# Kernel tuning notes

Hardware: AMD Instinct MI355X
Metric: run time of the kernel (lower is better)

## Reference

```python
import jax, jax.numpy as jnp
import numpy as np

H = 16          # num_attention_heads
D_MODEL = 2048  # hidden_size
HEAD_DIM = D_MODEL // H  # 128
B, S = 4, 2048


def setup_inputs() -> dict:
    key = jax.random.key(0)
    ks = jax.random.split(key, 9)
    std = D_MODEL ** -0.5
    hidden_states = jax.random.normal(ks[0], (B, S, D_MODEL), dtype=jnp.float32)
    q_w = jax.random.normal(ks[1], (H * HEAD_DIM, D_MODEL), dtype=jnp.float32) * std
    k_w = jax.random.normal(ks[2], (HEAD_DIM, D_MODEL), dtype=jnp.float32) * std
    v_w = jax.random.normal(ks[3], (HEAD_DIM, D_MODEL), dtype=jnp.float32) * std
    o_w = jax.random.normal(ks[4], (D_MODEL, H * HEAD_DIM), dtype=jnp.float32) * std
    q_b = jnp.zeros((H * HEAD_DIM,), dtype=jnp.float32)
    k_b = jnp.zeros((HEAD_DIM,), dtype=jnp.float32)
    v_b = jnp.zeros((HEAD_DIM,), dtype=jnp.float32)
    o_b = jnp.zeros((D_MODEL,), dtype=jnp.float32)
    return {"hidden_states": hidden_states, "q_w": q_w, "q_b": q_b,
            "k_w": k_w, "k_b": k_b, "v_w": v_w, "v_b": v_b,
            "o_w": o_w, "o_b": o_b}


def reference(hidden_states, q_w, q_b, k_w, k_b, v_w, v_b, o_w, o_b):
    b, s, _ = hidden_states.shape
    # projections: q -> H heads, k/v -> single shared KV head (MQA)
    q = (hidden_states @ q_w.T + q_b).reshape(b, s, H, HEAD_DIM)   # bshd
    k = hidden_states @ k_w.T + k_b                                 # bkd (1 kv head)
    v = hidden_states @ v_w.T + v_b                                 # bkd
    # QK^T with KV head broadcast across all query heads
    scores = jnp.einsum('bqhd,bkd->bhqk', q, k) / (HEAD_DIM ** 0.5)
    # causal mask (triu above diagonal)
    causal = jnp.triu(jnp.ones((s, s), dtype=bool), k=1)
    scores = jnp.where(causal[None, None], -jnp.inf, scores)
    # softmax in fp32, cast back to input dtype
    attn = jax.nn.softmax(scores.astype(jnp.float32), axis=-1).astype(q.dtype)
    out = jnp.einsum('bhqk,bkd->bqhd', attn, v).reshape(b, s, H * HEAD_DIM)
    return out @ o_w.T + o_b
```

## Files before the change

### kernel.cpp

```cpp
#include <hip/hip_runtime.h>
#include <stdint.h>

typedef __bf16 bf16;
typedef __bf16 bf16x4 __attribute__((ext_vector_type(4)));
typedef __bf16 bf16x8 __attribute__((ext_vector_type(8)));
typedef float f32x4 __attribute__((ext_vector_type(4)));
typedef short s16x4 __attribute__((ext_vector_type(4)));

using gp_t = __attribute__((address_space(1))) const void*;
using lp_t = __attribute__((address_space(3))) void*;

__device__ __forceinline__ void gld16(const void* g, void* l) {
  __builtin_amdgcn_global_load_lds((gp_t)g, (lp_t)l, 16, 0, 0);
}

struct CvtSegs {
  const float* src[10];
  bf16* dst[10];
  int cnt[10];
  int n;
};

__global__ void cvt_kernel(CvtSegs segs) {
  const int stride = gridDim.x * blockDim.x;
  const int t0 = blockIdx.x * blockDim.x + threadIdx.x;
  for (int s = 0; s < segs.n; s++) {
    const float4* src = (const float4*)segs.src[s];
    bf16x4* dst = (bf16x4*)segs.dst[s];
    int cnt4 = segs.cnt[s] >> 2;
    for (int idx = t0; idx < cnt4; idx += stride) {
      float4 v = src[idx];
      bf16x4 o; o[0] = (bf16)v.x; o[1] = (bf16)v.y; o[2] = (bf16)v.z; o[3] = (bf16)v.w;
      dst[idx] = o;
    }
  }
}

__global__ __launch_bounds__(256, 2)
void gemm_bt(const bf16* __restrict__ A, const void* __restrict__ Wv,
             const void* __restrict__ biasv, void* __restrict__ Cv,
             void* __restrict__ Cv2, void* __restrict__ Cv3,
             int M, int N, int K, int w_fp32, int bias_fp32, int store_sel)
{
  __shared__ __align__(16) bf16 As[128 * 64];
  __shared__ __align__(16) bf16 Bs[128 * 64];
  const int tid  = threadIdx.x;
  const int lane = tid & 63;
  const int w    = tid >> 6;
  const int wm   = w >> 1, wn = w & 1;
  const int quad = lane >> 4, l16 = lane & 15;
  const int m0 = blockIdx.x * 128, n0 = blockIdx.y * 128;

  f32x4 acc[4][4] = {};

  for (int k0 = 0; k0 < K; k0 += 64) {
#pragma unroll
    for (int it = 0; it < 4; it++) {
      int c = tid + it * 256;
      int row = c >> 3;
      int cc  = (c & 7) ^ (row & 7);
      gld16(A + (size_t)(m0 + row) * K + k0 + cc * 8, &As[c * 8]);
      size_t woff = (size_t)(n0 + row) * K + k0 + cc * 8;
      if (!w_fp32) {
        gld16((const bf16*)Wv + woff, &Bs[c * 8]);
      } else {
        const float* Wf = (const float*)Wv;
        float4 x0 = *(const float4*)(Wf + woff);
        float4 x1 = *(const float4*)(Wf + woff + 4);
        bf16x8 v;
        v[0] = (bf16)x0.x; v[1] = (bf16)x0.y; v[2] = (bf16)x0.z; v[3] = (bf16)x0.w;
        v[4] = (bf16)x1.x; v[5] = (bf16)x1.y; v[6] = (bf16)x1.z; v[7] = (bf16)x1.w;
        *(bf16x8*)&Bs[c * 8] = v;
      }
    }
    __syncthreads();
#pragma unroll
    for (int dk = 0; dk < 2; dk++) {
      bf16x8 af[4], bw[4];
#pragma unroll
      for (int i = 0; i < 4; i++) {
        int row = wm * 64 + i * 16 + l16;
        af[i] = *(const bf16x8*)&As[(row * 8 + ((dk * 4 + quad) ^ (row & 7))) * 8];
      }
#pragma unroll
      for (int j = 0; j < 4; j++) {
        int row = wn * 64 + j * 16 + l16;
        bw[j] = *(const bf16x8*)&Bs[(row * 8 + ((dk * 4 + quad) ^ (row & 7))) * 8];
      }
      __builtin_amdgcn_s_setprio(1);
#pragma unroll
      for (int i = 0; i < 4; i++)
#pragma unroll
        for (int j = 0; j < 4; j++)
          acc[i][j] = __builtin_amdgcn_mfma_f32_16x16x32_bf16(af[i], bw[j], acc[i][j], 0, 0, 0);
      __builtin_amdgcn_s_setprio(0);
    }
    __syncthreads();
  }

#pragma unroll
  for (int j = 0; j < 4; j++) {
    int col = n0 + wn * 64 + j * 16 + l16;
    float bv = bias_fp32 ? ((const float*)biasv)[col] : (float)((const bf16*)biasv)[col];
#pragma unroll
    for (int i = 0; i < 4; i++) {
#pragma unroll
      for (int r = 0; r < 4; r++) {
        int row = m0 + wm * 64 + i * 16 + quad * 4 + r;
        float v = acc[i][j][r] + bv;
        if (store_sel == 0) {
          ((bf16*)Cv)[(size_t)row * N + col] = (bf16)v;
        } else if (store_sel == 2) {
          ((float*)Cv)[(size_t)row * N + col] = v;
        } else {
          if (col < 2048) {
            ((bf16*)Cv)[(size_t)row * 2048 + col] = (bf16)v;
          } else if (col < 2176) {
            ((bf16*)Cv2)[(size_t)row * 128 + (col - 2048)] = (bf16)v;
          } else {
            int b = row >> 11, s = row & 2047;
            ((bf16*)Cv3)[((size_t)(b * 128 + (col - 2176))) * 2048 + s] = (bf16)v;
          }
        }
      }
    }
  }
}

__global__ __launch_bounds__(256, 2)
void mqa_attn(const bf16* Qg, const bf16* __restrict__ Kg,
              const bf16* __restrict__ Vtg, bf16* AO)
{
  __shared__ __align__(16) bf16 Ks[2][64 * 128];
  __shared__ __align__(16) bf16 Vs[2][128 * 64];

  const int tid  = threadIdx.x;
  const int lane = tid & 63;
  const int w    = tid >> 6;
  const int quad = lane >> 4, l16 = lane & 15;
  const int rb   = w * 32;
  const int bh = blockIdx.y;
  const int b  = bh >> 4, h = bh & 15;
  const float C2  = 0.12751879526288147f;
  const float NEG = -3.0e4f;

  for (int half = 0; half < 2; half++) {
    const int qi = half ? (15 - (int)blockIdx.x) : (int)blockIdx.x;
    const int q0 = qi * 128;

    bf16x8 aq[2][4];
    {
      const bf16* qb = Qg + ((size_t)(b * 2048 + q0 + rb + l16)) * 2048 + h * 128 + quad * 8;
#pragma unroll
      for (int i = 0; i < 2; i++)
#pragma unroll
        for (int dk = 0; dk < 4; dk++)
          aq[i][dk] = *(const bf16x8*)(qb + (size_t)i * 16 * 2048 + dk * 32);
    }

    float m_reg[2] = {NEG, NEG};
    float l_reg[2] = {0.0f, 0.0f};
    f32x4 ot[2][8] = {};

    const int nt = 2 * qi + 2;

#pragma unroll
    for (int it = 0; it < 4; it++) {
      int c = tid + it * 256;
      int rk = c >> 4, ck = (c & 15) ^ (rk & 15);
      gld16(Kg + ((size_t)(b * 2048 + rk)) * 128 + ck * 8, &Ks[0][c * 8]);
      int rv = c >> 3, cv = (c & 7) ^ (rv & 7);
      gld16(Vtg + ((size_t)(b * 128 + rv)) * 2048 + cv * 8, &Vs[0][c * 8]);
    }
    __syncthreads();

    int cur = 0;
    for (int kt = 0; kt < nt; kt++) {
      const int kk0 = kt * 64;

      if (kt + 1 < nt) {
        const int nk0 = kk0 + 64;
#pragma unroll
        for (int it = 0; it < 4; it++) {
          int c = tid + it * 256;
          int rk = c >> 4, ck = (c & 15) ^ (rk & 15);
          gld16(Kg + ((size_t)(b * 2048 + nk0 + rk)) * 128 + ck * 8, &Ks[cur ^ 1][c * 8]);
          int rv = c >> 3, cv = (c & 7) ^ (rv & 7);
          gld16(Vtg + ((size_t)(b * 128 + rv)) * 2048 + nk0 + cv * 8, &Vs[cur ^ 1][c * 8]);
        }
      }

      if (kk0 <= q0 + rb + 31) {
        f32x4 st[4][2] = {};
#pragma unroll
        for (int dk = 0; dk < 4; dk++) {
          bf16x8 bk[4];
#pragma unroll
          for (int j = 0; j < 4; j++) {
            int row = j * 16 + l16;
            bk[j] = *(const bf16x8*)&Ks[cur][(row * 16 + ((dk * 4 + quad) ^ (row & 15))) * 8];
          }
          __builtin_amdgcn_s_setprio(1);
#pragma unroll
          for (int j = 0; j < 4; j++)
#pragma unroll
            for (int i = 0; i < 2; i++)
              st[j][i] = __builtin_amdgcn_mfma_f32_16x16x32_bf16(bk[j], aq[i][dk], st[j][i], 0, 0, 0);
          __builtin_amdgcn_s_setprio(0);
        }

        if (kk0 + 63 > q0 + rb) {
#pragma unroll
          for (int j = 0; j < 4; j++)
#pragma unroll
            for (int i = 0; i < 2; i++)
#pragma unroll
              for (int r = 0; r < 4; r++) {
                int key = kk0 + j * 16 + quad * 4 + r;
                int qg  = q0 + rb + i * 16 + l16;
                if (key > qg) st[j][i][r] = NEG;
              }
        }

        s16x4 ps[2][4];
#pragma unroll
        for (int i = 0; i < 2; i++) {
          float mx = st[0][i][0];
#pragma unroll
          for (int j = 0; j < 4; j++)
#pragma unroll
            for (int r = 0; r < 4; r++) mx = fmaxf(mx, st[j][i][r]);
          mx = fmaxf(mx, __shfl_xor(mx, 16, 64));
          mx = fmaxf(mx, __shfl_xor(mx, 32, 64));
          float mo = m_reg[i];
          if (__any(mx > mo)) {
            float mn = fmaxf(mo, mx);
            float al = exp2f((mo - mn) * C2);
            l_reg[i] *= al;
#pragma unroll
            for (int jd = 0; jd < 8; jd++)
#pragma unroll
              for (int r = 0; r < 4; r++) ot[i][jd][r] *= al;
            m_reg[i] = mn;
          }
          float mc = m_reg[i] * C2;
          float rs = 0.0f;
#pragma unroll
          for (int j = 0; j < 4; j++) {
            float p0 = exp2f(st[j][i][0] * C2 - mc);
            float p1 = exp2f(st[j][i][1] * C2 - mc);
            float p2 = exp2f(st[j][i][2] * C2 - mc);
            float p3 = exp2f(st[j][i][3] * C2 - mc);
            rs += (p0 + p1) + (p2 + p3);
            union { bf16x4 h; s16x4 s; } pu;
            pu.h[0] = (bf16)p0; pu.h[1] = (bf16)p1;
            pu.h[2] = (bf16)p2; pu.h[3] = (bf16)p3;
            ps[i][j] = pu.s;
          }
          rs += __shfl_xor(rs, 16, 64);
          rs += __shfl_xor(rs, 32, 64);
          l_reg[i] += rs;
        }

#pragma unroll
        for (int jd = 0; jd < 8; jd++) {
          int vrow = jd * 16 + l16;
          s16x4 vf[4];
#pragma unroll
          for (int jk = 0; jk < 4; jk++) {
            int vch = (jk * 2 + (quad >> 1)) ^ (vrow & 7);
            vf[jk] = *(const s16x4*)&Vs[cur][(vrow * 8 + vch) * 8 + (quad & 1) * 4];
          }
          __builtin_amdgcn_s_setprio(1);
#pragma unroll
          for (int jk = 0; jk < 4; jk++)
#pragma unroll
            for (int i = 0; i < 2; i++)
              ot[i][jd] = __builtin_amdgcn_mfma_f32_16x16x16bf16_1k(vf[jk], ps[i][jk], ot[i][jd], 0, 0, 0);
          __builtin_amdgcn_s_setprio(0);
        }
      }
      __syncthreads();
      cur ^= 1;
    }

#pragma unroll
    for (int i = 0; i < 2; i++) {
      float l = l_reg[i];
      float inv = (l > 0.0f) ? 1.0f / l : 0.0f;
      size_t base = ((size_t)(b * 2048 + q0 + rb + i * 16 + l16)) * 2048 + h * 128 + quad * 4;
#pragma unroll
      for (int jd = 0; jd < 8; jd++) {
        bf16x4 ov;
#pragma unroll
        for (int r = 0; r < 4; r++) ov[r] = (bf16)(ot[i][jd][r] * inv);
        *(bf16x4*)(AO + base + jd * 16) = ov;
      }
    }
  }
}

extern "C" void kernel_launch(void* const* d_in, const int* in_sizes, int n_in,
                              void* d_out, int out_size, void* d_ws, size_t ws_size,
                              hipStream_t stream)
{
  const float* X   = (const float*)d_in[0];
  const float* q_w = (const float*)d_in[1];
  const float* q_b = (const float*)d_in[2];
  const float* k_w = (const float*)d_in[3];
  const float* k_b = (const float*)d_in[4];
  const float* v_w = (const float*)d_in[5];
  const float* v_b = (const float*)d_in[6];
  const float* o_w = (const float*)d_in[7];
  const float* o_b = (const float*)d_in[8];

  char* outc = (char*)d_out;
  bf16* Xb    = (bf16*)(outc);
  bf16* Kg    = (bf16*)(outc + 33554432);
  bf16* Vtg   = (bf16*)(outc + 35651584);
  bf16* wq_b  = (bf16*)(outc + 37748736);
  bf16* wkv_b = (bf16*)(outc + 46137344);
  bf16* qb_b  = (bf16*)(outc + 47185920);
  bf16* kvb_b = (bf16*)(outc + 47190016);

  bf16* Qg = (bf16*)d_ws;
  bf16* AO = Qg;

  const bool big_ws = ws_size >= (size_t)(33554432 + 8388608 + 8192);
  bf16* wo_b = big_ws ? (bf16*)((char*)d_ws + 33554432) : nullptr;
  bf16* ob_b = big_ws ? (bf16*)((char*)d_ws + 41943040) : nullptr;

  CvtSegs segs;
  int n = 0;
  segs.src[n] = X;   segs.dst[n] = Xb;            segs.cnt[n] = 16777216; n++;
  segs.src[n] = q_w; segs.dst[n] = wq_b;          segs.cnt[n] = 4194304;  n++;
  segs.src[n] = k_w; segs.dst[n] = wkv_b;         segs.cnt[n] = 262144;   n++;
  segs.src[n] = v_w; segs.dst[n] = wkv_b + 262144; segs.cnt[n] = 262144;  n++;
  segs.src[n] = q_b; segs.dst[n] = qb_b;          segs.cnt[n] = 2048;     n++;
  segs.src[n] = k_b; segs.dst[n] = kvb_b;         segs.cnt[n] = 128;      n++;
  segs.src[n] = v_b; segs.dst[n] = kvb_b + 128;   segs.cnt[n] = 128;      n++;
  if (big_ws) {
    segs.src[n] = o_w; segs.dst[n] = wo_b;        segs.cnt[n] = 4194304;  n++;
    segs.src[n] = o_b; segs.dst[n] = ob_b;        segs.cnt[n] = 2048;     n++;
  }
  segs.n = n;

  dim3 blk(256);
  cvt_kernel<<<dim3(1024), blk, 0, stream>>>(segs);
  gemm_bt<<<dim3(64, 18), blk, 0, stream>>>(Xb, wq_b, qb_b, Qg, Kg, Vtg,
                                            8192, 2304, 2048, 0, 0, 4);
  mqa_attn<<<dim3(8, 64), blk, 0, stream>>>(Qg, Kg, Vtg, AO);
  if (big_ws)
    gemm_bt<<<dim3(64, 16), blk, 0, stream>>>(AO, wo_b, ob_b, d_out, nullptr, nullptr,
                                              8192, 2048, 2048, 0, 0, 2);
  else
    gemm_bt<<<dim3(64, 16), blk, 0, stream>>>(AO, o_w, o_b, d_out, nullptr, nullptr,
                                              8192, 2048, 2048, 1, 1, 2);
}
```

Before: 488.6 us.

## Add double-buffered 256x256 GEMM kernel for QKV and output projections

Introduces a 512-thread GEMM with 256x256 output tiles and double-buffered LDS. Loads for the next K-step are interleaved with MFMA phases under explicit barriers. It replaces the 128x128 single-buffered GEMM for the fused QKV projection and the bf16-weight output projection, to raise operand reuse and hide global-load latency. The 128KB LDS footprint likely limits it to one block per CU. The QKV grid of 288 blocks may leave a mostly idle second wave on 256 CUs. The old kernel is kept, specialised, for the fp32-weight fallback.

```diff
diff --git a/kernel.cpp b/kernel.cpp
--- a/kernel.cpp
+++ b/kernel.cpp
@@ -36,11 +36,113 @@
   }
 }
 
+__global__ __launch_bounds__(512, 2)
+void gemm256(const bf16* __restrict__ A, const bf16* __restrict__ W,
+             const bf16* __restrict__ bias, void* __restrict__ Cv,
+             void* __restrict__ Cv2, void* __restrict__ Cv3,
+             int N, int K, int store_sel)
+{
+  __shared__ __align__(16) bf16 As[2][256 * 64];
+  __shared__ __align__(16) bf16 Bs[2][256 * 64];
+  const int tid  = threadIdx.x;
+  const int lane = tid & 63;
+  const int w    = tid >> 6;
+  const int wm   = w >> 2, wn = w & 3;
+  const int quad = lane >> 4, l16 = lane & 15;
+  const int m0 = blockIdx.x * 256, n0 = blockIdx.y * 256;
+
+  f32x4 acc[8][4] = {};
+
+  auto stageAB = [&](int buf, int k0, int itbase) {
+#pragma unroll
+    for (int it = itbase; it < itbase + 2; it++) {
+      int c   = tid + it * 512;
+      int row = c >> 3;
+      int cc  = (c & 7) ^ (row & 7);
+      gld16(A + (size_t)(m0 + row) * K + k0 + cc * 8, &As[buf][c * 8]);
+      gld16(W + (size_t)(n0 + row) * K + k0 + cc * 8, &Bs[buf][c * 8]);
+    }
+  };
+
+  stageAB(0, 0, 0);
+  stageAB(0, 0, 2);
+  __syncthreads();
+  __builtin_amdgcn_sched_barrier(0);
+
+  int cur = 0;
+  for (int k0 = 0; k0 < K; k0 += 64) {
+    const bool nxt = (k0 + 64 < K);
+    bf16x8 bw[4][2];
+#pragma unroll
+    for (int p = 0; p < 4; p++) {
+      if (nxt && p < 2) stageAB(cur ^ 1, k0 + 64, p * 2);
+      if (p == 0) {
+#pragma unroll
+        for (int nj = 0; nj < 4; nj++)
+#pragma unroll
+          for (int dk = 0; dk < 2; dk++) {
+            int row = wn * 64 + nj * 16 + l16;
+            bw[nj][dk] = *(const bf16x8*)&Bs[cur][(row * 8 + ((dk * 4 + quad) ^ (row & 7))) * 8];
+          }
+      }
+      bf16x8 af[2][2];
+#pragma unroll
+      for (int mi = 0; mi < 2; mi++)
+#pragma unroll
+        for (int dk = 0; dk < 2; dk++) {
+          int row = wm * 128 + (p * 2 + mi) * 16 + l16;
+          af[mi][dk] = *(const bf16x8*)&As[cur][(row * 8 + ((dk * 4 + quad) ^ (row & 7))) * 8];
+        }
+      __builtin_amdgcn_s_barrier();
+      __builtin_amdgcn_sched_barrier(0);
+      __builtin_amdgcn_s_setprio(1);
+#pragma unroll
+      for (int dk = 0; dk < 2; dk++)
+#pragma unroll
+        for (int mi = 0; mi < 2; mi++)
+#pragma unroll
+          for (int nj = 0; nj < 4; nj++)
+            acc[p * 2 + mi][nj] = __builtin_amdgcn_mfma_f32_16x16x32_bf16(
+                af[mi][dk], bw[nj][dk], acc[p * 2 + mi][nj], 0, 0, 0);
+      __builtin_amdgcn_s_setprio(0);
+      if (p == 3) asm volatile("s_waitcnt vmcnt(0)" ::: "memory");
+      __builtin_amdgcn_s_barrier();
+      __builtin_amdgcn_sched_barrier(0);
+    }
+    cur ^= 1;
+  }
+
+#pragma unroll
+  for (int nj = 0; nj < 4; nj++) {
+    int col = n0 + wn * 64 + nj * 16 + l16;
+    float bv = (float)bias[col];
+#pragma unroll
+    for (int mi = 0; mi < 8; mi++) {
+#pragma unroll
+      for (int r = 0; r < 4; r++) {
+        int row = m0 + wm * 128 + mi * 16 + quad * 4 + r;
+        float v = acc[mi][nj][r] + bv;
+        if (store_sel == 2) {
+          ((float*)Cv)[(size_t)row * N + col] = v;
+        } else {
+          if (col < 2048) {
+            ((bf16*)Cv)[(size_t)row * 2048 + col] = (bf16)v;
+          } else if (col < 2176) {
+            ((bf16*)Cv2)[(size_t)row * 128 + (col - 2048)] = (bf16)v;
+          } else {
+            int b = row >> 11, s = row & 2047;
+            ((bf16*)Cv3)[((size_t)(b * 128 + (col - 2176))) * 2048 + s] = (bf16)v;
+          }
+        }
+      }
+    }
+  }
+}
+
 __global__ __launch_bounds__(256, 2)
-void gemm_bt(const bf16* __restrict__ A, const void* __restrict__ Wv,
-             const void* __restrict__ biasv, void* __restrict__ Cv,
-             void* __restrict__ Cv2, void* __restrict__ Cv3,
-             int M, int N, int K, int w_fp32, int bias_fp32, int store_sel)
+void gemm_bt_f32w(const bf16* __restrict__ A, const float* __restrict__ Wf,
+                  const float* __restrict__ biasf, float* __restrict__ C,
+                  int M, int N, int K)
 {
   __shared__ __align__(16) bf16 As[128 * 64];
   __shared__ __align__(16) bf16 Bs[128 * 64];
@@ -61,17 +163,12 @@
       int cc  = (c & 7) ^ (row & 7);
       gld16(A + (size_t)(m0 + row) * K + k0 + cc * 8, &As[c * 8]);
       size_t woff = (size_t)(n0 + row) * K + k0 + cc * 8;
-      if (!w_fp32) {
-        gld16((const bf16*)Wv + woff, &Bs[c * 8]);
-      } else {
-        const float* Wf = (const float*)Wv;
-        float4 x0 = *(const float4*)(Wf + woff);
-        float4 x1 = *(const float4*)(Wf + woff + 4);
-        bf16x8 v;
-        v[0] = (bf16)x0.x; v[1] = (bf16)x0.y; v[2] = (bf16)x0.z; v[3] = (bf16)x0.w;
-        v[4] = (bf16)x1.x; v[5] = (bf16)x1.y; v[6] = (bf16)x1.z; v[7] = (bf16)x1.w;
-        *(bf16x8*)&Bs[c * 8] = v;
-      }
+      float4 x0 = *(const float4*)(Wf + woff);
+      float4 x1 = *(const float4*)(Wf + woff + 4);
+      bf16x8 v;
+      v[0] = (bf16)x0.x; v[1] = (bf16)x0.y; v[2] = (bf16)x0.z; v[3] = (bf16)x0.w;
+      v[4] = (bf16)x1.x; v[5] = (bf16)x1.y; v[6] = (bf16)x1.z; v[7] = (bf16)x1.w;
+      *(bf16x8*)&Bs[c * 8] = v;
     }
     __syncthreads();
 #pragma unroll
@@ -87,13 +184,11 @@
         int row = wn * 64 + j * 16 + l16;
         bw[j] = *(const bf16x8*)&Bs[(row * 8 + ((dk * 4 + quad) ^ (row & 7))) * 8];
       }
-      __builtin_amdgcn_s_setprio(1);
 #pragma unroll
       for (int i = 0; i < 4; i++)
 #pragma unroll
         for (int j = 0; j < 4; j++)
           acc[i][j] = __builtin_amdgcn_mfma_f32_16x16x32_bf16(af[i], bw[j], acc[i][j], 0, 0, 0);
-      __builtin_amdgcn_s_setprio(0);
     }
     __syncthreads();
   }
@@ -101,29 +196,14 @@
 #pragma unroll
   for (int j = 0; j < 4; j++) {
     int col = n0 + wn * 64 + j * 16 + l16;
-    float bv = bias_fp32 ? ((const float*)biasv)[col] : (float)((const bf16*)biasv)[col];
-#pragma unroll
-    for (int i = 0; i < 4; i++) {
+    float bv = biasf[col];
+#pragma unroll
+    for (int i = 0; i < 4; i++)
 #pragma unroll
       for (int r = 0; r < 4; r++) {
         int row = m0 + wm * 64 + i * 16 + quad * 4 + r;
-        float v = acc[i][j][r] + bv;
-        if (store_sel == 0) {
-          ((bf16*)Cv)[(size_t)row * N + col] = (bf16)v;
-        } else if (store_sel == 2) {
-          ((float*)Cv)[(size_t)row * N + col] = v;
-        } else {
-          if (col < 2048) {
-            ((bf16*)Cv)[(size_t)row * 2048 + col] = (bf16)v;
-          } else if (col < 2176) {
-            ((bf16*)Cv2)[(size_t)row * 128 + (col - 2048)] = (bf16)v;
-          } else {
-            int b = row >> 11, s = row & 2047;
-            ((bf16*)Cv3)[((size_t)(b * 128 + (col - 2176))) * 2048 + s] = (bf16)v;
-          }
-        }
-      }
-    }
+        C[(size_t)row * N + col] = acc[i][j][r] + bv;
+      }
   }
 }
 
@@ -345,15 +425,14 @@
   }
   segs.n = n;
 
-  dim3 blk(256);
-  cvt_kernel<<<dim3(1024), blk, 0, stream>>>(segs);
-  gemm_bt<<<dim3(64, 18), blk, 0, stream>>>(Xb, wq_b, qb_b, Qg, Kg, Vtg,
-                                            8192, 2304, 2048, 0, 0, 4);
-  mqa_attn<<<dim3(8, 64), blk, 0, stream>>>(Qg, Kg, Vtg, AO);
+  cvt_kernel<<<dim3(1024), dim3(256), 0, stream>>>(segs);
+  gemm256<<<dim3(32, 9), dim3(512), 0, stream>>>(Xb, wq_b, qb_b, Qg, Kg, Vtg,
+                                                 2304, 2048, 4);
+  mqa_attn<<<dim3(8, 64), dim3(256), 0, stream>>>(Qg, Kg, Vtg, AO);
   if (big_ws)
-    gemm_bt<<<dim3(64, 16), blk, 0, stream>>>(AO, wo_b, ob_b, d_out, nullptr, nullptr,
-                                              8192, 2048, 2048, 0, 0, 2);
+    gemm256<<<dim3(32, 8), dim3(512), 0, stream>>>(AO, wo_b, ob_b, d_out,
+                                                   nullptr, nullptr, 2048, 2048, 2);
   else
-    gemm_bt<<<dim3(64, 16), blk, 0, stream>>>(AO, o_w, o_b, d_out, nullptr, nullptr,
-                                              8192, 2048, 2048, 1, 1, 2);
-}
+    gemm_bt_f32w<<<dim3(64, 16), dim3(256), 0, stream>>>(AO, o_w, o_b, (float*)d_out,
+                                                         8192, 2048, 2048);
+}
```

After: 558.0 us. +14.2%, slower.
